# Kernel optimization log

Measured on AMD Instinct MI355X. Metric: run time of the kernel, lower is better.

The kernel has to match this reference:

```python
import jax, jax.numpy as jnp
import numpy as np


def setup_inputs() -> dict:
    key = jax.random.key(0)
    ks = jax.random.split(key, 8)
    B, L, I, H, O = 512, 512, 256, 1024, 1
    def glorot(k, shape, fan_sum):
        return jax.random.uniform(k, shape, jnp.float32, -1.0, 1.0) * (6.0 / fan_sum) ** 0.5
    return {
        "X": jax.random.normal(ks[0], (B, L, I), jnp.float32),
        "W_in1": glorot(ks[1], (H, I), H + I),
        "b_in1": jnp.zeros((H, 1), jnp.float32),
        "W_rec1": glorot(ks[2], (H, H), H + H),
        "W_in2": glorot(ks[3], (H, I), H + I),
        "b_in2": jnp.zeros((H, 1), jnp.float32),
        "W_rec2": glorot(ks[4], (H, H), H + H),
        "W_out": glorot(ks[5], (O, H), O + H),
        "b_out": jnp.zeros((O, 1), jnp.float32),
    }


def reference(X, W_in1, b_in1, W_rec1, W_in2, b_in2, W_rec2, W_out, b_out):
    B, L, I = X.shape
    H = W_in1.shape[0]
    Xs = jnp.swapaxes(X, 0, 1)  # (L, B, I)
    # Precompute the input-to-hidden projections for all timesteps (parallel GEMMs).
    in1 = jnp.einsum("hi,lbi->lbh", W_in1, Xs) + b_in1[:, 0]  # (L, B, H)
    in2 = jnp.einsum("hi,lbi->lbh", W_in2, Xs) + b_in2[:, 0]  # (L, B, H)
    even = (jnp.arange(L) % 2 == 0)[:, None, None]  # (L, 1, 1) broadcast mask

    def step(carry, xs):
        z12, z1, z2 = carry  # each (B, H)
        a1, a2, ev = xs
        z1n = jnp.tanh(a1 + z12 @ W_rec1.T)
        z2n = jnp.where(ev, jnp.tanh(a2 + z2 @ W_rec2.T), z2)  # branch updates only on even l
        return (z1n + z2n, z1n, z2n), None

    z0 = jnp.zeros((B, H), X.dtype)
    (z12, z1, z2), _ = jax.lax.scan(step, (z0, z0, z0), (in1, in2, even))
    z_out = jnp.tanh(z1 @ W_out.T + b_out[:, 0])  # (B, num_outputs)
    return z_out.reshape(B, 1)
```

## Files before the change

### kernel.cpp

```cpp
#include <hip/hip_runtime.h>
#include <hip/hip_bf16.h>

typedef __attribute__((ext_vector_type(8))) short bhalf8;
typedef __attribute__((ext_vector_type(4))) float fvec4;

static __device__ __forceinline__ unsigned short f2bf(float f) {
  unsigned u = __builtin_bit_cast(unsigned, f);
  u = (u + 0x7fffu + ((u >> 16) & 1u)) >> 16;
  return (unsigned short)u;
}
static __device__ __forceinline__ float tanh_fast(float x) {
  x = fminf(12.f, fmaxf(-12.f, x));
  float e = __expf(2.f * x);
  return (e - 1.f) / (e + 1.f);
}
static __device__ __forceinline__ fvec4 tanh4(fvec4 v) {
  fvec4 r;
  r[0] = tanh_fast(v[0]); r[1] = tanh_fast(v[1]);
  r[2] = tanh_fast(v[2]); r[3] = tanh_fast(v[3]);
  return r;
}
static __device__ __forceinline__ bhalf8 load_w8(const float* p) {
  fvec4 a = *(const fvec4*)p;
  fvec4 b = *(const fvec4*)(p + 4);
  bhalf8 r;
  r[0] = (short)f2bf(a[0]); r[1] = (short)f2bf(a[1]);
  r[2] = (short)f2bf(a[2]); r[3] = (short)f2bf(a[3]);
  r[4] = (short)f2bf(b[0]); r[5] = (short)f2bf(b[1]);
  r[6] = (short)f2bf(b[2]); r[7] = (short)f2bf(b[3]);
  return r;
}

static __device__ __forceinline__ void st_short_coh(unsigned short* p, unsigned v) {
  asm volatile("global_store_short %0, %1, off sc0 sc1" :: "v"(p), "v"(v) : "memory");
}
static __device__ __forceinline__ void st_f32_coh(float* p, float v) {
  asm volatile("global_store_dword %0, %1, off sc0 sc1" :: "v"(p), "v"(v) : "memory");
}
static __device__ __forceinline__ void st_u32_coh(unsigned* p, unsigned v) {
  asm volatile("global_store_dword %0, %1, off sc0 sc1" :: "v"(p), "v"(v) : "memory");
}
static __device__ __forceinline__ unsigned ld_u32_coh(const unsigned* p) {
  unsigned v;
  asm volatile("global_load_dword %0, %1, off sc0 sc1\n\ts_waitcnt vmcnt(0)"
               : "=v"(v) : "v"(p) : "memory");
  return v;
}
static __device__ __forceinline__ float ld_f32_coh(const float* p) {
  float v;
  asm volatile("global_load_dword %0, %1, off sc0 sc1\n\ts_waitcnt vmcnt(0)"
               : "=v"(v) : "v"(p) : "memory");
  return v;
}
static __device__ __forceinline__ void gll16_coh(const void* g, void* lds) {
  __builtin_amdgcn_global_load_lds(
      (const __attribute__((address_space(1))) void*)g,
      (__attribute__((address_space(3))) void*)lds, 16, 0, 0x11);
}

#define MFMA16(a, b, c) __builtin_amdgcn_mfma_f32_16x16x32_bf16((a), (b), (c), 0, 0, 0)

extern "C" __global__ void __launch_bounds__(256, 1)
alarm_rnn_persist(const float* __restrict__ X, const float* __restrict__ Win1,
                  const float* __restrict__ bin1, const float* __restrict__ Wrec1,
                  const float* __restrict__ Win2, const float* __restrict__ bin2,
                  const float* __restrict__ Wrec2, const float* __restrict__ Wout,
                  const float* __restrict__ bout, float* __restrict__ out,
                  unsigned* flags, unsigned short* gbuf0, unsigned short* gbuf1,
                  unsigned short* z2b0, unsigned short* z2b1, float* z1buf)
{
  constexpr int kL = 512, kI = 256, kH = 1024;
  extern __shared__ char smem[];

  const int tid = threadIdx.x, bid = blockIdx.x;
  const int grp = bid >> 4, memb = bid & 15;
  const int lane = tid & 63, w = tid >> 6;
  const int row16 = lane & 15, kq = lane >> 4;
  const int sw = (row16 & 7) << 4;
  const int hcol = memb * 64 + w * 16 + row16;
  const int brow0 = grp * 32;

  bhalf8 w1[32], w2[32], wi1[8], wi2[8];
  {
    const float* p1 = Wrec1 + (size_t)hcol * kH + kq * 8;
    const float* p2 = Wrec2 + (size_t)hcol * kH + kq * 8;
#pragma unroll
    for (int kk = 0; kk < 32; ++kk) {
      w1[kk] = load_w8(p1 + kk * 32);
      w2[kk] = load_w8(p2 + kk * 32);
    }
    const float* q1 = Win1 + (size_t)hcol * kI + kq * 8;
    const float* q2 = Win2 + (size_t)hcol * kI + kq * 8;
#pragma unroll
    for (int kk = 0; kk < 8; ++kk) {
      wi1[kk] = load_w8(q1 + kk * 32);
      wi2[kk] = load_w8(q2 + kk * 32);
    }
  }
  const float bv1 = bin1[hcol];
  const float bv2 = bin2[hcol];
  fvec4 z2c0 = {0.f, 0.f, 0.f, 0.f}, z2c1 = {0.f, 0.f, 0.f, 0.f};

  {
    int r = tid >> 3, q = tid & 7;
#pragma unroll
    for (int p = 0; p < 2; ++p) {
      const float* xp = X + (size_t)(brow0 + r) * (kL * kI) + (size_t)p * kI;
      fvec4 xv[8];
#pragma unroll
      for (int j = 0; j < 8; ++j) xv[j] = *(const fvec4*)(xp + q * 4 + j * 32);
#pragma unroll
      for (int j = 0; j < 8; ++j) {
        int i0 = q * 4 + j * 32;
        ushort4 pk;
        pk.x = f2bf(xv[j][0]); pk.y = f2bf(xv[j][1]);
        pk.z = f2bf(xv[j][2]); pk.w = f2bf(xv[j][3]);
        *(ushort4*)(smem + 131072 + p * 16384 + (r << 9) + ((i0 * 2) ^ ((r & 7) << 4))) = pk;
      }
    }
  }
  __syncthreads();

  for (int l = 0; l < kL; ++l) {
    const bool even = ((l & 1) == 0);
    const int e = l >> 1;

    {
      const unsigned short* zsrc = (l & 1) ? gbuf1 : gbuf0;
#pragma unroll
      for (int it = 0; it < 16; ++it) {
        int c = ((it * 4 + w) << 6) + lane;
        int r = c >> 7, cbs = (c & 127) * 16;
        gll16_coh((const char*)zsrc + (((size_t)(brow0 + r)) << 11) + (cbs ^ ((r & 7) << 4)),
                  smem + ((it * 4 + w) << 10));
      }
      if (even) {
        const unsigned short* z2src = (e & 1) ? z2b1 : z2b0;
#pragma unroll
        for (int it = 0; it < 16; ++it) {
          int c = ((it * 4 + w) << 6) + lane;
          int r = c >> 7, cbs = (c & 127) * 16;
          gll16_coh((const char*)z2src + (((size_t)(brow0 + r)) << 11) + (cbs ^ ((r & 7) << 4)),
                    smem + 65536 + ((it * 4 + w) << 10));
        }
      }
      __builtin_amdgcn_sched_barrier(0);
    }

    const char* xb = smem + 131072 + ((l & 1) << 14);
    fvec4 acc0 = {bv1, bv1, bv1, bv1}, acc1 = acc0;
#pragma unroll
    for (int kk = 0; kk < 8; ++kk) {
      int cb = kk * 64 + kq * 16;
      bhalf8 a0 = *(const bhalf8*)(xb + (row16 << 9) + (cb ^ sw));
      bhalf8 a1 = *(const bhalf8*)(xb + ((16 + row16) << 9) + (cb ^ sw));
      acc0 = MFMA16(a0, wi1[kk], acc0);
      acc1 = MFMA16(a1, wi1[kk], acc1);
    }
    fvec4 c2a0 = {bv2, bv2, bv2, bv2}, c2a1 = c2a0;
    if (even) {
#pragma unroll
      for (int kk = 0; kk < 8; ++kk) {
        int cb = kk * 64 + kq * 16;
        bhalf8 a0 = *(const bhalf8*)(xb + (row16 << 9) + (cb ^ sw));
        bhalf8 a1 = *(const bhalf8*)(xb + ((16 + row16) << 9) + (cb ^ sw));
        c2a0 = MFMA16(a0, wi2[kk], c2a0);
        c2a1 = MFMA16(a1, wi2[kk], c2a1);
      }
    }
    asm volatile("s_waitcnt vmcnt(0)" ::: "memory");
    __builtin_amdgcn_sched_barrier(0);
    __syncthreads();

#pragma unroll
    for (int kk = 0; kk < 32; ++kk) {
      int cb = kk * 64 + kq * 16;
      bhalf8 a0 = *(const bhalf8*)(smem + (row16 << 11) + (cb ^ sw));
      bhalf8 a1 = *(const bhalf8*)(smem + ((16 + row16) << 11) + (cb ^ sw));
      acc0 = MFMA16(a0, w1[kk], acc0);
      acc1 = MFMA16(a1, w1[kk], acc1);
    }
    fvec4 z1n0 = tanh4(acc0), z1n1 = tanh4(acc1);

    if (even) {
#pragma unroll
      for (int kk = 0; kk < 32; ++kk) {
        int cb = kk * 64 + kq * 16;
        bhalf8 a0 = *(const bhalf8*)(smem + 65536 + (row16 << 11) + (cb ^ sw));
        bhalf8 a1 = *(const bhalf8*)(smem + 65536 + ((16 + row16) << 11) + (cb ^ sw));
        c2a0 = MFMA16(a0, w2[kk], c2a0);
        c2a1 = MFMA16(a1, w2[kk], c2a1);
      }
      z2c0 = tanh4(c2a0);
      z2c1 = tanh4(c2a1);
    }

    if (l < kL - 1) {
      unsigned short* dst = (l & 1) ? gbuf0 : gbuf1;
#pragma unroll
      for (int i = 0; i < 4; ++i) {
        st_short_coh(dst + (size_t)(brow0 + kq * 4 + i) * kH + hcol, f2bf(z1n0[i] + z2c0[i]));
        st_short_coh(dst + (size_t)(brow0 + 16 + kq * 4 + i) * kH + hcol, f2bf(z1n1[i] + z2c1[i]));
      }
    } else {
#pragma unroll
      for (int i = 0; i < 4; ++i) {
        st_f32_coh(z1buf + (size_t)(brow0 + kq * 4 + i) * kH + hcol, z1n0[i]);
        st_f32_coh(z1buf + (size_t)(brow0 + 16 + kq * 4 + i) * kH + hcol, z1n1[i]);
      }
    }
    if (even) {
      unsigned short* z2dst = (e & 1) ? z2b0 : z2b1;
#pragma unroll
      for (int i = 0; i < 4; ++i) {
        st_short_coh(z2dst + (size_t)(brow0 + kq * 4 + i) * kH + hcol, f2bf(z2c0[i]));
        st_short_coh(z2dst + (size_t)(brow0 + 16 + kq * 4 + i) * kH + hcol, f2bf(z2c1[i]));
      }
    }
    asm volatile("s_waitcnt vmcnt(0)" ::: "memory");
    __syncthreads();
    if (tid == 0) st_u32_coh(flags + grp * 16 + memb, (unsigned)(l + 1));

    if (l + 2 < kL) {
      const int xr = tid >> 3, xq = tid & 7;
      const float* xp = X + (size_t)(brow0 + xr) * (kL * kI) + (size_t)(l + 2) * kI;
      fvec4 xv[8];
#pragma unroll
      for (int j = 0; j < 8; ++j) xv[j] = *(const fvec4*)(xp + xq * 4 + j * 32);
#pragma unroll
      for (int j = 0; j < 8; ++j) {
        int i0 = xq * 4 + j * 32;
        ushort4 pk;
        pk.x = f2bf(xv[j][0]); pk.y = f2bf(xv[j][1]);
        pk.z = f2bf(xv[j][2]); pk.w = f2bf(xv[j][3]);
        *(ushort4*)(smem + 131072 + ((l & 1) << 14) + (xr << 9) + ((i0 * 2) ^ ((xr & 7) << 4))) = pk;
      }
    }

    {
      const unsigned tgt = (unsigned)(l + 1);
      const unsigned* fp = flags + grp * 16 + (lane & 15);
      for (;;) {
        unsigned v = (lane < 16) ? ld_u32_coh(fp) : tgt;
        bool ok = (lane >= 16) || ((lane & 15) == memb) || (v >= tgt);
        if (__all(ok)) break;
        __builtin_amdgcn_s_sleep(1);
      }
      __builtin_amdgcn_sched_barrier(0);
    }
  }

  if (memb == 0) {
    int r = tid >> 3, q = tid & 7;
    const float* zr = z1buf + (size_t)(brow0 + r) * kH;
    float s = 0.f;
    for (int h = q * 128; h < q * 128 + 128; ++h) s += ld_f32_coh(zr + h) * Wout[h];
    s += __shfl_xor(s, 1);
    s += __shfl_xor(s, 2);
    s += __shfl_xor(s, 4);
    if (q == 0) out[brow0 + r] = tanh_fast(s + bout[0]);
  }
}

extern "C" void kernel_launch(void* const* d_in, const int* in_sizes, int n_in,
                              void* d_out, int out_size, void* d_ws, size_t ws_size,
                              hipStream_t stream) {
  const float* X = (const float*)d_in[0];
  const float* Win1 = (const float*)d_in[1];
  const float* bin1 = (const float*)d_in[2];
  const float* Wrec1 = (const float*)d_in[3];
  const float* Win2 = (const float*)d_in[4];
  const float* bin2 = (const float*)d_in[5];
  const float* Wrec2 = (const float*)d_in[6];
  const float* Wout = (const float*)d_in[7];
  const float* bout = (const float*)d_in[8];
  float* out = (float*)d_out;

  char* ws = (char*)d_ws;
  unsigned* flags = (unsigned*)ws;
  unsigned short* gbuf0 = (unsigned short*)(ws + 4096);
  unsigned short* gbuf1 = (unsigned short*)(ws + 4096 + (1 << 20));
  unsigned short* z2b0 = (unsigned short*)(ws + 4096 + (2 << 20));
  unsigned short* z2b1 = (unsigned short*)(ws + 4096 + (3 << 20));
  float* z1buf = (float*)(ws + 4096 + (4 << 20));

  (void)hipMemsetAsync(flags, 0, 4096, stream);
  (void)hipMemsetAsync(gbuf0, 0, (size_t)512 * 1024 * 2, stream);
  (void)hipMemsetAsync(z2b0, 0, (size_t)512 * 1024 * 2, stream);

  (void)hipFuncSetAttribute((const void*)alarm_rnn_persist,
                            hipFuncAttributeMaxDynamicSharedMemorySize, 163840);

  alarm_rnn_persist<<<dim3(256), dim3(256), 163840, stream>>>(
      X, Win1, bin1, Wrec1, Win2, bin2, Wrec2, Wout, bout, out,
      flags, gbuf0, gbuf1, z2b0, z2b1, z1buf);
}
```

Before: 6.382 ms.

## Repartition persistent RNN blocks to 16 rows by 128 hidden columns

Each block now covers 16 batch rows and 128 hidden columns using 512 threads, instead of 32 rows and 64 columns with 256 threads. Sync groups shrink from 16 to 8 blocks, so each flag poll checks fewer peers. X staging and the output reduction are reshaped to match, and LDS use drops to 96KB. The risk is register pressure: each wave still keeps all its recurrent and input weights in registers, while twice as many waves per CU and the (512,2) launch bound cut the per-wave register budget, which can force spills.

```diff
diff --git a/kernel.cpp b/kernel.cpp
--- a/kernel.cpp
+++ b/kernel.cpp
@@ -60,7 +60,7 @@
 
 #define MFMA16(a, b, c) __builtin_amdgcn_mfma_f32_16x16x32_bf16((a), (b), (c), 0, 0, 0)
 
-extern "C" __global__ void __launch_bounds__(256, 1)
+extern "C" __global__ void __launch_bounds__(512, 2)
 alarm_rnn_persist(const float* __restrict__ X, const float* __restrict__ Win1,
                   const float* __restrict__ bin1, const float* __restrict__ Wrec1,
                   const float* __restrict__ Win2, const float* __restrict__ bin2,
@@ -73,12 +73,12 @@
   extern __shared__ char smem[];
 
   const int tid = threadIdx.x, bid = blockIdx.x;
-  const int grp = bid >> 4, memb = bid & 15;
+  const int grp = bid >> 3, memb = bid & 7;
   const int lane = tid & 63, w = tid >> 6;
   const int row16 = lane & 15, kq = lane >> 4;
   const int sw = (row16 & 7) << 4;
-  const int hcol = memb * 64 + w * 16 + row16;
-  const int brow0 = grp * 32;
+  const int hcol = memb * 128 + w * 16 + row16;
+  const int brow0 = grp * 16;
 
   bhalf8 w1[32], w2[32], wi1[8], wi2[8];
   {
@@ -99,24 +99,21 @@
   }
   const float bv1 = bin1[hcol];
   const float bv2 = bin2[hcol];
-  fvec4 z2c0 = {0.f, 0.f, 0.f, 0.f}, z2c1 = {0.f, 0.f, 0.f, 0.f};
+  fvec4 z2c0 = {0.f, 0.f, 0.f, 0.f};
 
   {
-    int r = tid >> 3, q = tid & 7;
+    int r = tid >> 5, q = tid & 31;
 #pragma unroll
     for (int p = 0; p < 2; ++p) {
-      const float* xp = X + (size_t)(brow0 + r) * (kL * kI) + (size_t)p * kI;
-      fvec4 xv[8];
-#pragma unroll
-      for (int j = 0; j < 8; ++j) xv[j] = *(const fvec4*)(xp + q * 4 + j * 32);
-#pragma unroll
-      for (int j = 0; j < 8; ++j) {
-        int i0 = q * 4 + j * 32;
-        ushort4 pk;
-        pk.x = f2bf(xv[j][0]); pk.y = f2bf(xv[j][1]);
-        pk.z = f2bf(xv[j][2]); pk.w = f2bf(xv[j][3]);
-        *(ushort4*)(smem + 131072 + p * 16384 + (r << 9) + ((i0 * 2) ^ ((r & 7) << 4))) = pk;
-      }
+      const float* xp = X + (size_t)(brow0 + r) * (kL * kI) + (size_t)p * kI + q * 8;
+      fvec4 a = *(const fvec4*)xp;
+      fvec4 b = *(const fvec4*)(xp + 4);
+      ushort4 lo, hi;
+      lo.x = f2bf(a[0]); lo.y = f2bf(a[1]); lo.z = f2bf(a[2]); lo.w = f2bf(a[3]);
+      hi.x = f2bf(b[0]); hi.y = f2bf(b[1]); hi.z = f2bf(b[2]); hi.w = f2bf(b[3]);
+      char* dp = smem + 65536 + p * 8192 + (r << 9) + ((q << 4) ^ ((r & 7) << 4));
+      *(ushort4*)dp = lo;
+      *(ushort4*)(dp + 8) = hi;
     }
   }
   __syncthreads();
@@ -128,44 +125,40 @@
     {
       const unsigned short* zsrc = (l & 1) ? gbuf1 : gbuf0;
 #pragma unroll
-      for (int it = 0; it < 16; ++it) {
-        int c = ((it * 4 + w) << 6) + lane;
+      for (int it = 0; it < 4; ++it) {
+        int c = ((it * 8 + w) << 6) + lane;
         int r = c >> 7, cbs = (c & 127) * 16;
         gll16_coh((const char*)zsrc + (((size_t)(brow0 + r)) << 11) + (cbs ^ ((r & 7) << 4)),
-                  smem + ((it * 4 + w) << 10));
+                  smem + ((it * 8 + w) << 10));
       }
       if (even) {
         const unsigned short* z2src = (e & 1) ? z2b1 : z2b0;
 #pragma unroll
-        for (int it = 0; it < 16; ++it) {
-          int c = ((it * 4 + w) << 6) + lane;
+        for (int it = 0; it < 4; ++it) {
+          int c = ((it * 8 + w) << 6) + lane;
           int r = c >> 7, cbs = (c & 127) * 16;
           gll16_coh((const char*)z2src + (((size_t)(brow0 + r)) << 11) + (cbs ^ ((r & 7) << 4)),
-                    smem + 65536 + ((it * 4 + w) << 10));
+                    smem + 32768 + ((it * 8 + w) << 10));
         }
       }
       __builtin_amdgcn_sched_barrier(0);
     }
 
-    const char* xb = smem + 131072 + ((l & 1) << 14);
-    fvec4 acc0 = {bv1, bv1, bv1, bv1}, acc1 = acc0;
+    const char* xb = smem + 65536 + ((l & 1) << 13);
+    fvec4 acc0 = {bv1, bv1, bv1, bv1};
 #pragma unroll
     for (int kk = 0; kk < 8; ++kk) {
       int cb = kk * 64 + kq * 16;
       bhalf8 a0 = *(const bhalf8*)(xb + (row16 << 9) + (cb ^ sw));
-      bhalf8 a1 = *(const bhalf8*)(xb + ((16 + row16) << 9) + (cb ^ sw));
       acc0 = MFMA16(a0, wi1[kk], acc0);
-      acc1 = MFMA16(a1, wi1[kk], acc1);
-    }
-    fvec4 c2a0 = {bv2, bv2, bv2, bv2}, c2a1 = c2a0;
+    }
+    fvec4 c2a0 = {bv2, bv2, bv2, bv2};
     if (even) {
 #pragma unroll
       for (int kk = 0; kk < 8; ++kk) {
         int cb = kk * 64 + kq * 16;
         bhalf8 a0 = *(const bhalf8*)(xb + (row16 << 9) + (cb ^ sw));
-        bhalf8 a1 = *(const bhalf8*)(xb + ((16 + row16) << 9) + (cb ^ sw));
         c2a0 = MFMA16(a0, wi2[kk], c2a0);
-        c2a1 = MFMA16(a1, wi2[kk], c2a1);
       }
     }
     asm volatile("s_waitcnt vmcnt(0)" ::: "memory");
@@ -176,73 +169,59 @@
     for (int kk = 0; kk < 32; ++kk) {
       int cb = kk * 64 + kq * 16;
       bhalf8 a0 = *(const bhalf8*)(smem + (row16 << 11) + (cb ^ sw));
-      bhalf8 a1 = *(const bhalf8*)(smem + ((16 + row16) << 11) + (cb ^ sw));
       acc0 = MFMA16(a0, w1[kk], acc0);
-      acc1 = MFMA16(a1, w1[kk], acc1);
-    }
-    fvec4 z1n0 = tanh4(acc0), z1n1 = tanh4(acc1);
+    }
+    fvec4 z1n0 = tanh4(acc0);
 
     if (even) {
 #pragma unroll
       for (int kk = 0; kk < 32; ++kk) {
         int cb = kk * 64 + kq * 16;
-        bhalf8 a0 = *(const bhalf8*)(smem + 65536 + (row16 << 11) + (cb ^ sw));
-        bhalf8 a1 = *(const bhalf8*)(smem + 65536 + ((16 + row16) << 11) + (cb ^ sw));
+        bhalf8 a0 = *(const bhalf8*)(smem + 32768 + (row16 << 11) + (cb ^ sw));
         c2a0 = MFMA16(a0, w2[kk], c2a0);
-        c2a1 = MFMA16(a1, w2[kk], c2a1);
       }
       z2c0 = tanh4(c2a0);
-      z2c1 = tanh4(c2a1);
     }
 
     if (l < kL - 1) {
       unsigned short* dst = (l & 1) ? gbuf0 : gbuf1;
 #pragma unroll
-      for (int i = 0; i < 4; ++i) {
+      for (int i = 0; i < 4; ++i)
         st_short_coh(dst + (size_t)(brow0 + kq * 4 + i) * kH + hcol, f2bf(z1n0[i] + z2c0[i]));
-        st_short_coh(dst + (size_t)(brow0 + 16 + kq * 4 + i) * kH + hcol, f2bf(z1n1[i] + z2c1[i]));
-      }
     } else {
 #pragma unroll
-      for (int i = 0; i < 4; ++i) {
+      for (int i = 0; i < 4; ++i)
         st_f32_coh(z1buf + (size_t)(brow0 + kq * 4 + i) * kH + hcol, z1n0[i]);
-        st_f32_coh(z1buf + (size_t)(brow0 + 16 + kq * 4 + i) * kH + hcol, z1n1[i]);
-      }
     }
     if (even) {
       unsigned short* z2dst = (e & 1) ? z2b0 : z2b1;
 #pragma unroll
-      for (int i = 0; i < 4; ++i) {
+      for (int i = 0; i < 4; ++i)
         st_short_coh(z2dst + (size_t)(brow0 + kq * 4 + i) * kH + hcol, f2bf(z2c0[i]));
-        st_short_coh(z2dst + (size_t)(brow0 + 16 + kq * 4 + i) * kH + hcol, f2bf(z2c1[i]));
-      }
     }
     asm volatile("s_waitcnt vmcnt(0)" ::: "memory");
     __syncthreads();
-    if (tid == 0) st_u32_coh(flags + grp * 16 + memb, (unsigned)(l + 1));
+    if (tid == 0) st_u32_coh(flags + grp * 8 + memb, (unsigned)(l + 1));
 
     if (l + 2 < kL) {
-      const int xr = tid >> 3, xq = tid & 7;
-      const float* xp = X + (size_t)(brow0 + xr) * (kL * kI) + (size_t)(l + 2) * kI;
-      fvec4 xv[8];
-#pragma unroll
-      for (int j = 0; j < 8; ++j) xv[j] = *(const fvec4*)(xp + xq * 4 + j * 32);
-#pragma unroll
-      for (int j = 0; j < 8; ++j) {
-        int i0 = xq * 4 + j * 32;
-        ushort4 pk;
-        pk.x = f2bf(xv[j][0]); pk.y = f2bf(xv[j][1]);
-        pk.z = f2bf(xv[j][2]); pk.w = f2bf(xv[j][3]);
-        *(ushort4*)(smem + 131072 + ((l & 1) << 14) + (xr << 9) + ((i0 * 2) ^ ((xr & 7) << 4))) = pk;
-      }
+      int r = tid >> 5, q = tid & 31;
+      const float* xp = X + (size_t)(brow0 + r) * (kL * kI) + (size_t)(l + 2) * kI + q * 8;
+      fvec4 a = *(const fvec4*)xp;
+      fvec4 b = *(const fvec4*)(xp + 4);
+      ushort4 lo, hi;
+      lo.x = f2bf(a[0]); lo.y = f2bf(a[1]); lo.z = f2bf(a[2]); lo.w = f2bf(a[3]);
+      hi.x = f2bf(b[0]); hi.y = f2bf(b[1]); hi.z = f2bf(b[2]); hi.w = f2bf(b[3]);
+      char* dp = smem + 65536 + ((l & 1) << 13) + (r << 9) + ((q << 4) ^ ((r & 7) << 4));
+      *(ushort4*)dp = lo;
+      *(ushort4*)(dp + 8) = hi;
     }
 
     {
       const unsigned tgt = (unsigned)(l + 1);
-      const unsigned* fp = flags + grp * 16 + (lane & 15);
+      const unsigned* fp = flags + grp * 8 + (lane & 7);
       for (;;) {
-        unsigned v = (lane < 16) ? ld_u32_coh(fp) : tgt;
-        bool ok = (lane >= 16) || ((lane & 15) == memb) || (v >= tgt);
+        unsigned v = (lane < 8) ? ld_u32_coh(fp) : tgt;
+        bool ok = (lane >= 8) || ((lane & 7) == memb) || (v >= tgt);
         if (__all(ok)) break;
         __builtin_amdgcn_s_sleep(1);
       }
@@ -251,13 +230,15 @@
   }
 
   if (memb == 0) {
-    int r = tid >> 3, q = tid & 7;
+    int r = tid >> 5, q = tid & 31;
     const float* zr = z1buf + (size_t)(brow0 + r) * kH;
     float s = 0.f;
-    for (int h = q * 128; h < q * 128 + 128; ++h) s += ld_f32_coh(zr + h) * Wout[h];
+    for (int h = q * 32; h < q * 32 + 32; ++h) s += ld_f32_coh(zr + h) * Wout[h];
     s += __shfl_xor(s, 1);
     s += __shfl_xor(s, 2);
     s += __shfl_xor(s, 4);
+    s += __shfl_xor(s, 8);
+    s += __shfl_xor(s, 16);
     if (q == 0) out[brow0 + r] = tanh_fast(s + bout[0]);
   }
 }
@@ -289,9 +270,9 @@
   (void)hipMemsetAsync(z2b0, 0, (size_t)512 * 1024 * 2, stream);
 
   (void)hipFuncSetAttribute((const void*)alarm_rnn_persist,
-                            hipFuncAttributeMaxDynamicSharedMemorySize, 163840);
-
-  alarm_rnn_persist<<<dim3(256), dim3(256), 163840, stream>>>(
+                            hipFuncAttributeMaxDynamicSharedMemorySize, 98304);
+
+  alarm_rnn_persist<<<dim3(256), dim3(512), 98304, stream>>>(
       X, Win1, bin1, Wrec1, Win2, bin2, Wrec2, Wout, bout, out,
       flags, gbuf0, gbuf1, z2b0, z2b1, z1buf);
 }
```

New measurement: 8.752 ms. 1.37x slower.

## Map batch groups to single XCDs and exchange hidden state through L2

Applied to the files above, without the earlier changes.

Block IDs are remapped so the 16 blocks of each batch group land on one XCD, assuming round-robin dispatch of blocks across 8 XCDs. At startup each block records its XCC_ID and checks whether its whole group shares an XCD. If so, it uses plain stores and sc0-only loads that stay in the shared L2, instead of system-coherent sc0 sc1 traffic and direct-to-LDS loads, and overlaps the state loads with the input MFMAs. This targets cross-block state-exchange latency on each recurrent step. It adds a startup handshake, and if blocks are spread across XCDs it falls back to the old path.

```diff
diff --git a/kernel.cpp b/kernel.cpp
--- a/kernel.cpp
+++ b/kernel.cpp
@@ -3,6 +3,7 @@
 
 typedef __attribute__((ext_vector_type(8))) short bhalf8;
 typedef __attribute__((ext_vector_type(4))) float fvec4;
+typedef __attribute__((ext_vector_type(4))) unsigned u32x4;
 
 static __device__ __forceinline__ unsigned short f2bf(float f) {
   unsigned u = __builtin_bit_cast(unsigned, f);
@@ -34,11 +35,19 @@
 static __device__ __forceinline__ void st_short_coh(unsigned short* p, unsigned v) {
   asm volatile("global_store_short %0, %1, off sc0 sc1" :: "v"(p), "v"(v) : "memory");
 }
+static __device__ __forceinline__ void st_short_l2(unsigned short* p, unsigned v) {
+  asm volatile("global_store_short %0, %1, off" :: "v"(p), "v"(v) : "memory");
+}
 static __device__ __forceinline__ void st_f32_coh(float* p, float v) {
   asm volatile("global_store_dword %0, %1, off sc0 sc1" :: "v"(p), "v"(v) : "memory");
 }
 static __device__ __forceinline__ void st_u32_coh(unsigned* p, unsigned v) {
   asm volatile("global_store_dword %0, %1, off sc0 sc1" :: "v"(p), "v"(v) : "memory");
+}
+static __device__ __forceinline__ u32x4 ld16_l2(const void* p) {
+  u32x4 v;
+  asm volatile("global_load_dwordx4 %0, %1, off sc0" : "=v"(v) : "v"(p) : "memory");
+  return v;
 }
 static __device__ __forceinline__ unsigned ld_u32_coh(const unsigned* p) {
   unsigned v;
@@ -66,14 +75,20 @@
                   const float* __restrict__ Win2, const float* __restrict__ bin2,
                   const float* __restrict__ Wrec2, const float* __restrict__ Wout,
                   const float* __restrict__ bout, float* __restrict__ out,
-                  unsigned* flags, unsigned short* gbuf0, unsigned short* gbuf1,
+                  unsigned* sync, unsigned short* gbuf0, unsigned short* gbuf1,
                   unsigned short* z2b0, unsigned short* z2b1, float* z1buf)
 {
   constexpr int kL = 512, kI = 256, kH = 1024;
   extern __shared__ char smem[];
 
+  unsigned* flags = sync;
+  unsigned* pflags = sync + 256;
+  unsigned* xcds = sync + 512;
+
   const int tid = threadIdx.x, bid = blockIdx.x;
-  const int grp = bid >> 4, memb = bid & 15;
+  const int slot = bid >> 3;
+  const int grp = (bid & 7) * 2 + (slot >> 4);
+  const int memb = slot & 15;
   const int lane = tid & 63, w = tid >> 6;
   const int row16 = lane & 15, kq = lane >> 4;
   const int sw = (row16 & 7) << 4;
@@ -100,6 +115,29 @@
   const float bv1 = bin1[hcol];
   const float bv2 = bin2[hcol];
   fvec4 z2c0 = {0.f, 0.f, 0.f, 0.f}, z2c1 = {0.f, 0.f, 0.f, 0.f};
+
+  unsigned myxcd;
+  asm volatile("s_getreg_b32 %0, hwreg(HW_REG_XCC_ID)" : "=s"(myxcd));
+  myxcd &= 0xF;
+  if (tid == 0) {
+    st_u32_coh(xcds + grp * 16 + memb, myxcd);
+    asm volatile("s_waitcnt vmcnt(0)" ::: "memory");
+    st_u32_coh(pflags + grp * 16 + memb, 1u);
+  }
+  {
+    const unsigned* fp = pflags + grp * 16 + (lane & 15);
+    for (;;) {
+      unsigned v = (lane < 16) ? ld_u32_coh(fp) : 1u;
+      bool ok = (lane >= 16) || (v >= 1u);
+      if (__all(ok)) break;
+      __builtin_amdgcn_s_sleep(1);
+    }
+  }
+  bool l2m;
+  {
+    unsigned v = (lane < 16) ? ld_u32_coh(xcds + grp * 16 + (lane & 15)) : myxcd;
+    l2m = __all(v == myxcd);
+  }
 
   {
     int r = tid >> 3, q = tid & 7;
@@ -124,9 +162,65 @@
   for (int l = 0; l < kL; ++l) {
     const bool even = ((l & 1) == 0);
     const int e = l >> 1;
-
-    {
-      const unsigned short* zsrc = (l & 1) ? gbuf1 : gbuf0;
+    const unsigned short* zsrc = (l & 1) ? gbuf1 : gbuf0;
+    const unsigned short* z2src = (e & 1) ? z2b1 : z2b0;
+    const char* xb = smem + 131072 + ((l & 1) << 14);
+
+    fvec4 acc0 = {bv1, bv1, bv1, bv1}, acc1 = acc0;
+    fvec4 c2a0 = {bv2, bv2, bv2, bv2}, c2a1 = c2a0;
+
+    if (l2m) {
+      u32x4 ztmp[16];
+#pragma unroll
+      for (int it = 0; it < 16; ++it) {
+        int c = it * 256 + tid;
+        int r = c >> 7, cb = (c & 127) * 16;
+        ztmp[it] = ld16_l2((const char*)zsrc + (((size_t)(brow0 + r)) << 11) + cb);
+      }
+#pragma unroll
+      for (int kk = 0; kk < 8; ++kk) {
+        int cb = kk * 64 + kq * 16;
+        bhalf8 a0 = *(const bhalf8*)(xb + (row16 << 9) + (cb ^ sw));
+        bhalf8 a1 = *(const bhalf8*)(xb + ((16 + row16) << 9) + (cb ^ sw));
+        acc0 = MFMA16(a0, wi1[kk], acc0);
+        acc1 = MFMA16(a1, wi1[kk], acc1);
+      }
+      __builtin_amdgcn_sched_barrier(0);
+      asm volatile("s_waitcnt vmcnt(0)" ::: "memory");
+      __builtin_amdgcn_sched_barrier(0);
+#pragma unroll
+      for (int it = 0; it < 16; ++it) {
+        int c = it * 256 + tid;
+        int r = c >> 7, cb = (c & 127) * 16;
+        *(u32x4*)(smem + (r << 11) + (cb ^ ((r & 7) << 4))) = ztmp[it];
+      }
+      if (even) {
+        u32x4 z2t[16];
+#pragma unroll
+        for (int it = 0; it < 16; ++it) {
+          int c = it * 256 + tid;
+          int r = c >> 7, cb = (c & 127) * 16;
+          z2t[it] = ld16_l2((const char*)z2src + (((size_t)(brow0 + r)) << 11) + cb);
+        }
+#pragma unroll
+        for (int kk = 0; kk < 8; ++kk) {
+          int cb = kk * 64 + kq * 16;
+          bhalf8 a0 = *(const bhalf8*)(xb + (row16 << 9) + (cb ^ sw));
+          bhalf8 a1 = *(const bhalf8*)(xb + ((16 + row16) << 9) + (cb ^ sw));
+          c2a0 = MFMA16(a0, wi2[kk], c2a0);
+          c2a1 = MFMA16(a1, wi2[kk], c2a1);
+        }
+        __builtin_amdgcn_sched_barrier(0);
+        asm volatile("s_waitcnt vmcnt(0)" ::: "memory");
+        __builtin_amdgcn_sched_barrier(0);
+#pragma unroll
+        for (int it = 0; it < 16; ++it) {
+          int c = it * 256 + tid;
+          int r = c >> 7, cb = (c & 127) * 16;
+          *(u32x4*)(smem + 65536 + (r << 11) + (cb ^ ((r & 7) << 4))) = z2t[it];
+        }
+      }
+    } else {
 #pragma unroll
       for (int it = 0; it < 16; ++it) {
         int c = ((it * 4 + w) << 6) + lane;
@@ -135,7 +229,6 @@
                   smem + ((it * 4 + w) << 10));
       }
       if (even) {
-        const unsigned short* z2src = (e & 1) ? z2b1 : z2b0;
 #pragma unroll
         for (int it = 0; it < 16; ++it) {
           int c = ((it * 4 + w) << 6) + lane;
@@ -145,31 +238,27 @@
         }
       }
       __builtin_amdgcn_sched_barrier(0);
-    }
-
-    const char* xb = smem + 131072 + ((l & 1) << 14);
-    fvec4 acc0 = {bv1, bv1, bv1, bv1}, acc1 = acc0;
-#pragma unroll
-    for (int kk = 0; kk < 8; ++kk) {
-      int cb = kk * 64 + kq * 16;
-      bhalf8 a0 = *(const bhalf8*)(xb + (row16 << 9) + (cb ^ sw));
-      bhalf8 a1 = *(const bhalf8*)(xb + ((16 + row16) << 9) + (cb ^ sw));
-      acc0 = MFMA16(a0, wi1[kk], acc0);
-      acc1 = MFMA16(a1, wi1[kk], acc1);
-    }
-    fvec4 c2a0 = {bv2, bv2, bv2, bv2}, c2a1 = c2a0;
-    if (even) {
 #pragma unroll
       for (int kk = 0; kk < 8; ++kk) {
         int cb = kk * 64 + kq * 16;
         bhalf8 a0 = *(const bhalf8*)(xb + (row16 << 9) + (cb ^ sw));
         bhalf8 a1 = *(const bhalf8*)(xb + ((16 + row16) << 9) + (cb ^ sw));
-        c2a0 = MFMA16(a0, wi2[kk], c2a0);
-        c2a1 = MFMA16(a1, wi2[kk], c2a1);
-      }
-    }
-    asm volatile("s_waitcnt vmcnt(0)" ::: "memory");
-    __builtin_amdgcn_sched_barrier(0);
+        acc0 = MFMA16(a0, wi1[kk], acc0);
+        acc1 = MFMA16(a1, wi1[kk], acc1);
+      }
+      if (even) {
+#pragma unroll
+        for (int kk = 0; kk < 8; ++kk) {
+          int cb = kk * 64 + kq * 16;
+          bhalf8 a0 = *(const bhalf8*)(xb + (row16 << 9) + (cb ^ sw));
+          bhalf8 a1 = *(const bhalf8*)(xb + ((16 + row16) << 9) + (cb ^ sw));
+          c2a0 = MFMA16(a0, wi2[kk], c2a0);
+          c2a1 = MFMA16(a1, wi2[kk], c2a1);
+        }
+      }
+      asm volatile("s_waitcnt vmcnt(0)" ::: "memory");
+      __builtin_amdgcn_sched_barrier(0);
+    }
     __syncthreads();
 
 #pragma unroll
@@ -197,10 +286,18 @@
 
     if (l < kL - 1) {
       unsigned short* dst = (l & 1) ? gbuf0 : gbuf1;
-#pragma unroll
-      for (int i = 0; i < 4; ++i) {
-        st_short_coh(dst + (size_t)(brow0 + kq * 4 + i) * kH + hcol, f2bf(z1n0[i] + z2c0[i]));
-        st_short_coh(dst + (size_t)(brow0 + 16 + kq * 4 + i) * kH + hcol, f2bf(z1n1[i] + z2c1[i]));
+      if (l2m) {
+#pragma unroll
+        for (int i = 0; i < 4; ++i) {
+          st_short_l2(dst + (size_t)(brow0 + kq * 4 + i) * kH + hcol, f2bf(z1n0[i] + z2c0[i]));
+          st_short_l2(dst + (size_t)(brow0 + 16 + kq * 4 + i) * kH + hcol, f2bf(z1n1[i] + z2c1[i]));
+        }
+      } else {
+#pragma unroll
+        for (int i = 0; i < 4; ++i) {
+          st_short_coh(dst + (size_t)(brow0 + kq * 4 + i) * kH + hcol, f2bf(z1n0[i] + z2c0[i]));
+          st_short_coh(dst + (size_t)(brow0 + 16 + kq * 4 + i) * kH + hcol, f2bf(z1n1[i] + z2c1[i]));
+        }
       }
     } else {
 #pragma unroll
@@ -211,10 +308,18 @@
     }
     if (even) {
       unsigned short* z2dst = (e & 1) ? z2b0 : z2b1;
-#pragma unroll
-      for (int i = 0; i < 4; ++i) {
-        st_short_coh(z2dst + (size_t)(brow0 + kq * 4 + i) * kH + hcol, f2bf(z2c0[i]));
-        st_short_coh(z2dst + (size_t)(brow0 + 16 + kq * 4 + i) * kH + hcol, f2bf(z2c1[i]));
+      if (l2m) {
+#pragma unroll
+        for (int i = 0; i < 4; ++i) {
+          st_short_l2(z2dst + (size_t)(brow0 + kq * 4 + i) * kH + hcol, f2bf(z2c0[i]));
+          st_short_l2(z2dst + (size_t)(brow0 + 16 + kq * 4 + i) * kH + hcol, f2bf(z2c1[i]));
+        }
+      } else {
+#pragma unroll
+        for (int i = 0; i < 4; ++i) {
+          st_short_coh(z2dst + (size_t)(brow0 + kq * 4 + i) * kH + hcol, f2bf(z2c0[i]));
+          st_short_coh(z2dst + (size_t)(brow0 + 16 + kq * 4 + i) * kH + hcol, f2bf(z2c1[i]));
+        }
       }
     }
     asm volatile("s_waitcnt vmcnt(0)" ::: "memory");
@@ -277,14 +382,14 @@
   float* out = (float*)d_out;
 
   char* ws = (char*)d_ws;
-  unsigned* flags = (unsigned*)ws;
+  unsigned* sync = (unsigned*)ws;
   unsigned short* gbuf0 = (unsigned short*)(ws + 4096);
   unsigned short* gbuf1 = (unsigned short*)(ws + 4096 + (1 << 20));
   unsigned short* z2b0 = (unsigned short*)(ws + 4096 + (2 << 20));
   unsigned short* z2b1 = (unsigned short*)(ws + 4096 + (3 << 20));
   float* z1buf = (float*)(ws + 4096 + (4 << 20));
 
-  (void)hipMemsetAsync(flags, 0, 4096, stream);
+  (void)hipMemsetAsync(sync, 0, 4096, stream);
   (void)hipMemsetAsync(gbuf0, 0, (size_t)512 * 1024 * 2, stream);
   (void)hipMemsetAsync(z2b0, 0, (size_t)512 * 1024 * 2, stream);
 
@@ -293,5 +398,5 @@
 
   alarm_rnn_persist<<<dim3(256), dim3(256), 163840, stream>>>(
       X, Win1, bin1, Wrec1, Win2, bin2, Wrec2, Wout, bout, out,
-      flags, gbuf0, gbuf1, z2b0, z2b1, z1buf);
-}
+      sync, gbuf0, gbuf1, z2b0, z2b1, z1buf);
+}
```

New measurement: 8.980 ms. 40.7% more time.

## Split batch rows into two half-groups and ping-pong to overlap sync with compute

Applied to the files above, without the earlier changes.

Each workgroup's 32 batch rows are split into two 16-row halves, each with its own flag set. While one half computes, the other half's cross-block barrier wait and hidden-state loads are in flight, so the inter-block synchronisation latency is meant to hide behind MFMA work. Outputs are first transposed through LDS and written to global memory as 16-byte coherent stores instead of scattered 2-byte stores. In exchange there are more __syncthreads per step, two separate polling phases, and twice as many flag arrays, which assumes the workspace has room for them.

```diff
diff --git a/kernel.cpp b/kernel.cpp
--- a/kernel.cpp
+++ b/kernel.cpp
@@ -3,6 +3,7 @@
 
 typedef __attribute__((ext_vector_type(8))) short bhalf8;
 typedef __attribute__((ext_vector_type(4))) float fvec4;
+typedef __attribute__((ext_vector_type(4))) unsigned u32x4;
 
 static __device__ __forceinline__ unsigned short f2bf(float f) {
   unsigned u = __builtin_bit_cast(unsigned, f);
@@ -31,14 +32,14 @@
   return r;
 }
 
-static __device__ __forceinline__ void st_short_coh(unsigned short* p, unsigned v) {
-  asm volatile("global_store_short %0, %1, off sc0 sc1" :: "v"(p), "v"(v) : "memory");
-}
 static __device__ __forceinline__ void st_f32_coh(float* p, float v) {
   asm volatile("global_store_dword %0, %1, off sc0 sc1" :: "v"(p), "v"(v) : "memory");
 }
 static __device__ __forceinline__ void st_u32_coh(unsigned* p, unsigned v) {
   asm volatile("global_store_dword %0, %1, off sc0 sc1" :: "v"(p), "v"(v) : "memory");
+}
+static __device__ __forceinline__ void st16_coh(void* p, u32x4 v) {
+  asm volatile("global_store_dwordx4 %0, %1, off sc0 sc1" :: "v"(p), "v"(v) : "memory");
 }
 static __device__ __forceinline__ unsigned ld_u32_coh(const unsigned* p) {
   unsigned v;
@@ -59,6 +60,19 @@
 }
 
 #define MFMA16(a, b, c) __builtin_amdgcn_mfma_f32_16x16x32_bf16((a), (b), (c), 0, 0, 0)
+
+#define POLL(base, tgtv)                                                     \
+  {                                                                          \
+    const unsigned tgt_ = (unsigned)(tgtv);                                  \
+    const unsigned* fp_ = (base) + (lane & 15);                              \
+    for (;;) {                                                               \
+      unsigned v_ = (lane < 16) ? ld_u32_coh(fp_) : tgt_;                    \
+      bool ok_ = (lane >= 16) || ((lane & 15) == memb) || (v_ >= tgt_);      \
+      if (__all(ok_)) break;                                                 \
+      __builtin_amdgcn_s_sleep(1);                                           \
+    }                                                                        \
+    __builtin_amdgcn_sched_barrier(0);                                       \
+  }
 
 extern "C" __global__ void __launch_bounds__(256, 1)
 alarm_rnn_persist(const float* __restrict__ X, const float* __restrict__ Win1,
@@ -71,6 +85,12 @@
 {
   constexpr int kL = 512, kI = 256, kH = 1024;
   extern __shared__ char smem[];
+  char* zA = smem;
+  char* zB = smem + 32768;
+  char* z2A = smem + 65536;
+  char* z2B = smem + 98304;
+  char* xA = smem + 131072;
+  char* xB = smem + 147456;
 
   const int tid = threadIdx.x, bid = blockIdx.x;
   const int grp = bid >> 4, memb = bid & 15;
@@ -78,7 +98,9 @@
   const int row16 = lane & 15, kq = lane >> 4;
   const int sw = (row16 & 7) << 4;
   const int hcol = memb * 64 + w * 16 + row16;
-  const int brow0 = grp * 32;
+  const int rbA = grp * 32, rbB = grp * 32 + 16;
+  unsigned* flagsA = flags + grp * 16;
+  unsigned* flagsB = flags + 256 + grp * 16;
 
   bhalf8 w1[32], w2[32], wi1[8], wi2[8];
   {
@@ -99,166 +121,190 @@
   }
   const float bv1 = bin1[hcol];
   const float bv2 = bin2[hcol];
-  fvec4 z2c0 = {0.f, 0.f, 0.f, 0.f}, z2c1 = {0.f, 0.f, 0.f, 0.f};
-
-  {
-    int r = tid >> 3, q = tid & 7;
-#pragma unroll
-    for (int p = 0; p < 2; ++p) {
-      const float* xp = X + (size_t)(brow0 + r) * (kL * kI) + (size_t)p * kI;
-      fvec4 xv[8];
-#pragma unroll
-      for (int j = 0; j < 8; ++j) xv[j] = *(const fvec4*)(xp + q * 4 + j * 32);
-#pragma unroll
-      for (int j = 0; j < 8; ++j) {
-        int i0 = q * 4 + j * 32;
-        ushort4 pk;
-        pk.x = f2bf(xv[j][0]); pk.y = f2bf(xv[j][1]);
-        pk.z = f2bf(xv[j][2]); pk.w = f2bf(xv[j][3]);
-        *(ushort4*)(smem + 131072 + p * 16384 + (r << 9) + ((i0 * 2) ^ ((r & 7) << 4))) = pk;
-      }
-    }
-  }
+  fvec4 z2cA = {0.f, 0.f, 0.f, 0.f}, z2cB = {0.f, 0.f, 0.f, 0.f};
+
+  auto stage_x = [&](int rb, int step, char* dst) {
+    int r = tid >> 4, t = tid & 15;
+    const float* xp = X + (size_t)(rb + r) * (kL * kI) + (size_t)step * kI;
+#pragma unroll
+    for (int j = 0; j < 4; ++j) {
+      fvec4 v = *(const fvec4*)(xp + t * 4 + j * 64);
+      ushort4 pk;
+      pk.x = f2bf(v[0]); pk.y = f2bf(v[1]); pk.z = f2bf(v[2]); pk.w = f2bf(v[3]);
+      int i0 = t * 4 + j * 64;
+      *(ushort4*)(dst + (r << 9) + ((i0 * 2) ^ ((r & 7) << 4))) = pk;
+    }
+  };
+  auto stage_z = [&](const unsigned short* src, int rb, char* dst) {
+#pragma unroll
+    for (int it = 0; it < 8; ++it) {
+      int ci = (((it + memb) & 7) * 4) + w;
+      int r = ci >> 1, colb = (ci & 1) * 1024 + lane * 16;
+      gll16_coh((const char*)src + (((size_t)(rb + r)) << 11) + (colb ^ ((r & 7) << 4)),
+                dst + ci * 1024 + lane * 16);
+    }
+  };
+
+  stage_x(rbA, 0, xA); stage_x(rbA, 1, xA + 8192);
+  stage_x(rbB, 0, xB); stage_x(rbB, 1, xB + 8192);
+  stage_z(gbuf0, rbA, zA);
+  stage_z(z2b0, rbA, z2A);
+  asm volatile("s_waitcnt vmcnt(0)" ::: "memory");
   __syncthreads();
 
   for (int l = 0; l < kL; ++l) {
-    const bool even = ((l & 1) == 0);
-    const int e = l >> 1;
-
+    const bool ev = ((l & 1) == 0);
+
+    if (l > 0) POLL(flagsB, l);
     {
-      const unsigned short* zsrc = (l & 1) ? gbuf1 : gbuf0;
-#pragma unroll
-      for (int it = 0; it < 16; ++it) {
-        int c = ((it * 4 + w) << 6) + lane;
-        int r = c >> 7, cbs = (c & 127) * 16;
-        gll16_coh((const char*)zsrc + (((size_t)(brow0 + r)) << 11) + (cbs ^ ((r & 7) << 4)),
-                  smem + ((it * 4 + w) << 10));
-      }
-      if (even) {
-        const unsigned short* z2src = (e & 1) ? z2b1 : z2b0;
-#pragma unroll
-        for (int it = 0; it < 16; ++it) {
-          int c = ((it * 4 + w) << 6) + lane;
-          int r = c >> 7, cbs = (c & 127) * 16;
-          gll16_coh((const char*)z2src + (((size_t)(brow0 + r)) << 11) + (cbs ^ ((r & 7) << 4)),
-                    smem + 65536 + ((it * 4 + w) << 10));
-        }
-      }
+      stage_z((l & 1) ? gbuf1 : gbuf0, rbB, zB);
+      if (ev) stage_z(((l >> 1) & 1) ? z2b1 : z2b0, rbB, z2B);
       __builtin_amdgcn_sched_barrier(0);
     }
-
-    const char* xb = smem + 131072 + ((l & 1) << 14);
-    fvec4 acc0 = {bv1, bv1, bv1, bv1}, acc1 = acc0;
-#pragma unroll
-    for (int kk = 0; kk < 8; ++kk) {
-      int cb = kk * 64 + kq * 16;
-      bhalf8 a0 = *(const bhalf8*)(xb + (row16 << 9) + (cb ^ sw));
-      bhalf8 a1 = *(const bhalf8*)(xb + ((16 + row16) << 9) + (cb ^ sw));
-      acc0 = MFMA16(a0, wi1[kk], acc0);
-      acc1 = MFMA16(a1, wi1[kk], acc1);
-    }
-    fvec4 c2a0 = {bv2, bv2, bv2, bv2}, c2a1 = c2a0;
-    if (even) {
+    {
+      const char* xb = xA + ((l & 1) << 13);
+      fvec4 acc = {bv1, bv1, bv1, bv1};
 #pragma unroll
       for (int kk = 0; kk < 8; ++kk) {
         int cb = kk * 64 + kq * 16;
-        bhalf8 a0 = *(const bhalf8*)(xb + (row16 << 9) + (cb ^ sw));
-        bhalf8 a1 = *(const bhalf8*)(xb + ((16 + row16) << 9) + (cb ^ sw));
-        c2a0 = MFMA16(a0, wi2[kk], c2a0);
-        c2a1 = MFMA16(a1, wi2[kk], c2a1);
-      }
-    }
-    asm volatile("s_waitcnt vmcnt(0)" ::: "memory");
-    __builtin_amdgcn_sched_barrier(0);
-    __syncthreads();
-
-#pragma unroll
-    for (int kk = 0; kk < 32; ++kk) {
-      int cb = kk * 64 + kq * 16;
-      bhalf8 a0 = *(const bhalf8*)(smem + (row16 << 11) + (cb ^ sw));
-      bhalf8 a1 = *(const bhalf8*)(smem + ((16 + row16) << 11) + (cb ^ sw));
-      acc0 = MFMA16(a0, w1[kk], acc0);
-      acc1 = MFMA16(a1, w1[kk], acc1);
-    }
-    fvec4 z1n0 = tanh4(acc0), z1n1 = tanh4(acc1);
-
-    if (even) {
+        acc = MFMA16(*(const bhalf8*)(xb + (row16 << 9) + (cb ^ sw)), wi1[kk], acc);
+      }
+      fvec4 c2a = {bv2, bv2, bv2, bv2};
+      if (ev) {
+#pragma unroll
+        for (int kk = 0; kk < 8; ++kk) {
+          int cb = kk * 64 + kq * 16;
+          c2a = MFMA16(*(const bhalf8*)(xb + (row16 << 9) + (cb ^ sw)), wi2[kk], c2a);
+        }
+      }
 #pragma unroll
       for (int kk = 0; kk < 32; ++kk) {
         int cb = kk * 64 + kq * 16;
-        bhalf8 a0 = *(const bhalf8*)(smem + 65536 + (row16 << 11) + (cb ^ sw));
-        bhalf8 a1 = *(const bhalf8*)(smem + 65536 + ((16 + row16) << 11) + (cb ^ sw));
-        c2a0 = MFMA16(a0, w2[kk], c2a0);
-        c2a1 = MFMA16(a1, w2[kk], c2a1);
-      }
-      z2c0 = tanh4(c2a0);
-      z2c1 = tanh4(c2a1);
-    }
-
-    if (l < kL - 1) {
-      unsigned short* dst = (l & 1) ? gbuf0 : gbuf1;
-#pragma unroll
-      for (int i = 0; i < 4; ++i) {
-        st_short_coh(dst + (size_t)(brow0 + kq * 4 + i) * kH + hcol, f2bf(z1n0[i] + z2c0[i]));
-        st_short_coh(dst + (size_t)(brow0 + 16 + kq * 4 + i) * kH + hcol, f2bf(z1n1[i] + z2c1[i]));
-      }
-    } else {
-#pragma unroll
-      for (int i = 0; i < 4; ++i) {
-        st_f32_coh(z1buf + (size_t)(brow0 + kq * 4 + i) * kH + hcol, z1n0[i]);
-        st_f32_coh(z1buf + (size_t)(brow0 + 16 + kq * 4 + i) * kH + hcol, z1n1[i]);
-      }
-    }
-    if (even) {
-      unsigned short* z2dst = (e & 1) ? z2b0 : z2b1;
-#pragma unroll
-      for (int i = 0; i < 4; ++i) {
-        st_short_coh(z2dst + (size_t)(brow0 + kq * 4 + i) * kH + hcol, f2bf(z2c0[i]));
-        st_short_coh(z2dst + (size_t)(brow0 + 16 + kq * 4 + i) * kH + hcol, f2bf(z2c1[i]));
-      }
-    }
-    asm volatile("s_waitcnt vmcnt(0)" ::: "memory");
-    __syncthreads();
-    if (tid == 0) st_u32_coh(flags + grp * 16 + memb, (unsigned)(l + 1));
-
-    if (l + 2 < kL) {
-      const int xr = tid >> 3, xq = tid & 7;
-      const float* xp = X + (size_t)(brow0 + xr) * (kL * kI) + (size_t)(l + 2) * kI;
-      fvec4 xv[8];
-#pragma unroll
-      for (int j = 0; j < 8; ++j) xv[j] = *(const fvec4*)(xp + xq * 4 + j * 32);
-#pragma unroll
-      for (int j = 0; j < 8; ++j) {
-        int i0 = xq * 4 + j * 32;
-        ushort4 pk;
-        pk.x = f2bf(xv[j][0]); pk.y = f2bf(xv[j][1]);
-        pk.z = f2bf(xv[j][2]); pk.w = f2bf(xv[j][3]);
-        *(ushort4*)(smem + 131072 + ((l & 1) << 14) + (xr << 9) + ((i0 * 2) ^ ((xr & 7) << 4))) = pk;
-      }
-    }
-
+        acc = MFMA16(*(const bhalf8*)(zA + (row16 << 11) + (cb ^ sw)), w1[kk], acc);
+      }
+      fvec4 z1n = tanh4(acc);
+      if (ev) {
+#pragma unroll
+        for (int kk = 0; kk < 32; ++kk) {
+          int cb = kk * 64 + kq * 16;
+          c2a = MFMA16(*(const bhalf8*)(z2A + (row16 << 11) + (cb ^ sw)), w2[kk], c2a);
+        }
+        z2cA = tanh4(c2a);
+      }
+      __syncthreads();
+      if (l < kL - 1) {
+        const int colb2 = (w * 16 + row16) * 2;
+#pragma unroll
+        for (int i = 0; i < 4; ++i) {
+          int r0 = kq * 4 + i;
+          *(unsigned short*)(zA + r0 * 128 + (colb2 ^ ((r0 & 7) << 4))) = f2bf(z1n[i] + z2cA[i]);
+          if (ev)
+            *(unsigned short*)(zA + 2048 + r0 * 128 + (colb2 ^ ((r0 & 7) << 4))) = f2bf(z2cA[i]);
+        }
+        __syncthreads();
+        if (tid < 128) {
+          int r = tid >> 3, s = tid & 7;
+          u32x4 v = *(const u32x4*)(zA + r * 128 + ((s * 16) ^ ((r & 7) << 4)));
+          unsigned short* dst = (l & 1) ? gbuf0 : gbuf1;
+          st16_coh((char*)dst + (((size_t)(rbA + r)) << 11) + memb * 128 + s * 16, v);
+          if (ev) {
+            u32x4 v2 = *(const u32x4*)(zA + 2048 + r * 128 + ((s * 16) ^ ((r & 7) << 4)));
+            unsigned short* z2dst = ((l >> 1) & 1) ? z2b0 : z2b1;
+            st16_coh((char*)z2dst + (((size_t)(rbA + r)) << 11) + memb * 128 + s * 16, v2);
+          }
+        }
+      } else {
+#pragma unroll
+        for (int i = 0; i < 4; ++i)
+          st_f32_coh(z1buf + (size_t)(rbA + kq * 4 + i) * kH + hcol, z1n[i]);
+      }
+      asm volatile("s_waitcnt vmcnt(0)" ::: "memory");
+      __syncthreads();
+      if (tid == 0) st_u32_coh(flagsA + memb, (unsigned)(l + 1));
+      if (l + 2 < kL) stage_x(rbA, l + 2, xA + ((l & 1) << 13));
+    }
+
+    if (l + 1 < kL) {
+      POLL(flagsA, l + 1);
+      stage_z(((l + 1) & 1) ? gbuf1 : gbuf0, rbA, zA);
+      if (((l + 1) & 1) == 0) stage_z((((l + 1) >> 1) & 1) ? z2b1 : z2b0, rbA, z2A);
+      __builtin_amdgcn_sched_barrier(0);
+    }
     {
-      const unsigned tgt = (unsigned)(l + 1);
-      const unsigned* fp = flags + grp * 16 + (lane & 15);
-      for (;;) {
-        unsigned v = (lane < 16) ? ld_u32_coh(fp) : tgt;
-        bool ok = (lane >= 16) || ((lane & 15) == memb) || (v >= tgt);
-        if (__all(ok)) break;
-        __builtin_amdgcn_s_sleep(1);
-      }
-      __builtin_amdgcn_sched_barrier(0);
+      const char* xb = xB + ((l & 1) << 13);
+      fvec4 acc = {bv1, bv1, bv1, bv1};
+#pragma unroll
+      for (int kk = 0; kk < 8; ++kk) {
+        int cb = kk * 64 + kq * 16;
+        acc = MFMA16(*(const bhalf8*)(xb + (row16 << 9) + (cb ^ sw)), wi1[kk], acc);
+      }
+      fvec4 c2a = {bv2, bv2, bv2, bv2};
+      if (ev) {
+#pragma unroll
+        for (int kk = 0; kk < 8; ++kk) {
+          int cb = kk * 64 + kq * 16;
+          c2a = MFMA16(*(const bhalf8*)(xb + (row16 << 9) + (cb ^ sw)), wi2[kk], c2a);
+        }
+      }
+#pragma unroll
+      for (int kk = 0; kk < 32; ++kk) {
+        int cb = kk * 64 + kq * 16;
+        acc = MFMA16(*(const bhalf8*)(zB + (row16 << 11) + (cb ^ sw)), w1[kk], acc);
+      }
+      fvec4 z1n = tanh4(acc);
+      if (ev) {
+#pragma unroll
+        for (int kk = 0; kk < 32; ++kk) {
+          int cb = kk * 64 + kq * 16;
+          c2a = MFMA16(*(const bhalf8*)(z2B + (row16 << 11) + (cb ^ sw)), w2[kk], c2a);
+        }
+        z2cB = tanh4(c2a);
+      }
+      __syncthreads();
+      if (l < kL - 1) {
+        const int colb2 = (w * 16 + row16) * 2;
+#pragma unroll
+        for (int i = 0; i < 4; ++i) {
+          int r0 = kq * 4 + i;
+          *(unsigned short*)(zB + r0 * 128 + (colb2 ^ ((r0 & 7) << 4))) = f2bf(z1n[i] + z2cB[i]);
+          if (ev)
+            *(unsigned short*)(zB + 2048 + r0 * 128 + (colb2 ^ ((r0 & 7) << 4))) = f2bf(z2cB[i]);
+        }
+        __syncthreads();
+        if (tid < 128) {
+          int r = tid >> 3, s = tid & 7;
+          u32x4 v = *(const u32x4*)(zB + r * 128 + ((s * 16) ^ ((r & 7) << 4)));
+          unsigned short* dst = (l & 1) ? gbuf0 : gbuf1;
+          st16_coh((char*)dst + (((size_t)(rbB + r)) << 11) + memb * 128 + s * 16, v);
+          if (ev) {
+            u32x4 v2 = *(const u32x4*)(zB + 2048 + r * 128 + ((s * 16) ^ ((r & 7) << 4)));
+            unsigned short* z2dst = ((l >> 1) & 1) ? z2b0 : z2b1;
+            st16_coh((char*)z2dst + (((size_t)(rbB + r)) << 11) + memb * 128 + s * 16, v2);
+          }
+        }
+      } else {
+#pragma unroll
+        for (int i = 0; i < 4; ++i)
+          st_f32_coh(z1buf + (size_t)(rbB + kq * 4 + i) * kH + hcol, z1n[i]);
+      }
+      asm volatile("s_waitcnt vmcnt(0)" ::: "memory");
+      __syncthreads();
+      if (tid == 0) st_u32_coh(flagsB + memb, (unsigned)(l + 1));
+      if (l + 2 < kL) stage_x(rbB, l + 2, xB + ((l & 1) << 13));
     }
   }
 
   if (memb == 0) {
+    POLL(flagsA, kL);
+    POLL(flagsB, kL);
     int r = tid >> 3, q = tid & 7;
-    const float* zr = z1buf + (size_t)(brow0 + r) * kH;
+    const float* zr = z1buf + (size_t)(grp * 32 + r) * kH;
     float s = 0.f;
     for (int h = q * 128; h < q * 128 + 128; ++h) s += ld_f32_coh(zr + h) * Wout[h];
     s += __shfl_xor(s, 1);
     s += __shfl_xor(s, 2);
     s += __shfl_xor(s, 4);
-    if (q == 0) out[brow0 + r] = tanh_fast(s + bout[0]);
+    if (q == 0) out[grp * 32 + r] = tanh_fast(s + bout[0]);
   }
 }
 
```

Result: slower. 7.698 ms (+20.6%).
